# Optimization experiments

Hardware: AMD Instinct MI355X
Metric: run time of the kernel (lower is better)

Reference implementation:

```python
import jax, jax.numpy as jnp
import numpy as np

B, D, N, F = 2048, 512, 100000, 64
NEG = -1000000.0


def setup_inputs() -> dict:
    key = jax.random.key(0)
    k1, k2, k3, k4 = jax.random.split(key, 4)
    q = jax.random.normal(k1, (B, D), dtype=jnp.float32)
    rhs = jax.random.normal(k2, (D, N), dtype=jnp.float32)
    queries = jax.random.randint(k3, (B, 3), 0, N, dtype=jnp.int64)
    filter_idx = jax.random.randint(k4, (B, F), 0, N, dtype=jnp.int64)
    return {"q": q, "rhs": rhs, "queries": queries, "filter_idx": filter_idx}


def reference(q, rhs, queries, filter_idx):
    # targets[i] = score of the true triple = q[i] . rhs[:, true_rhs[i]]
    true_rhs = queries[:, 2]                         # [B]
    targets = jnp.einsum('bd,bd->b', q, rhs[:, true_rhs].T)  # [B]

    scores = q @ rhs                                  # [B, N]

    # filtered ranking: mask out known true tails + the query's own tail
    rows = jnp.arange(scores.shape[0])[:, None]       # [B, 1]
    scores = scores.at[rows, filter_idx].set(NEG)
    scores = scores.at[jnp.arange(scores.shape[0]), true_rhs].set(NEG)

    # rank = 1 + number of candidates scoring >= the true triple
    ranks = 1.0 + jnp.sum((scores >= targets[:, None]).astype(jnp.float32), axis=1)
    return ranks
```

## Files before the change

kernel.cpp:

```cpp
#include <hip/hip_runtime.h>
#include <hip/hip_bf16.h>

#define B_ 2048
#define D_ 512
#define N_ 100000
#define F_ 64
#define NEGV (-1000000.0f)

typedef __bf16 bfx8 __attribute__((ext_vector_type(8)));
typedef float f32x4 __attribute__((ext_vector_type(4)));
typedef unsigned short u16x8 __attribute__((ext_vector_type(8)));

static __device__ __forceinline__ unsigned short f2bf(float f) {
  unsigned u = __float_as_uint(f);
  unsigned r = (u + 0x7fffu + ((u >> 16) & 1u)) >> 16;
  return (unsigned short)r;
}
static __device__ __forceinline__ float bf2f(unsigned short u) {
  return __uint_as_float(((unsigned)u) << 16);
}

static __device__ __forceinline__ void async_copy16(const void* g, void* l) {
  __builtin_amdgcn_global_load_lds((const __attribute__((address_space(1))) void*)g,
                                   (__attribute__((address_space(3))) void*)l, 16, 0, 0);
}

__global__ void targets_init(const float* __restrict__ q, const float* __restrict__ rhs,
                             const int* __restrict__ queries, float* __restrict__ targets,
                             float* __restrict__ out) {
  __shared__ float wsum[4];
  int b = blockIdx.x;
  int tid = threadIdx.x, lane = tid & 63, w = tid >> 6;
  int p = queries[b * 3 + 2];
  float s = 0.f;
  for (int d = tid; d < D_; d += 256) s += q[b * D_ + d] * rhs[(size_t)d * N_ + p];
  for (int off = 32; off; off >>= 1) s += __shfl_down(s, off, 64);
  if (lane == 0) wsum[w] = s;
  __syncthreads();
  if (tid == 0) {
    targets[b] = wsum[0] + wsum[1] + wsum[2] + wsum[3];
    out[b] = 1.0f;
  }
}

__global__ void convert_q(const float* __restrict__ q, unsigned short* __restrict__ qb) {
  int i = blockIdx.x * blockDim.x + threadIdx.x;
  const float4* q4 = (const float4*)q;
  float4 v = q4[i];
  ushort4 o;
  o.x = f2bf(v.x); o.y = f2bf(v.y); o.z = f2bf(v.z); o.w = f2bf(v.w);
  ((ushort4*)qb)[i] = o;
}

__global__ void transpose_rhs(const float* __restrict__ rhs, unsigned short* __restrict__ rt) {
  __shared__ float tile[64][65];
  int n0 = blockIdx.x * 64, d0 = blockIdx.y * 64;
  int c = threadIdx.x & 63, r4 = threadIdx.x >> 6;
#pragma unroll
  for (int p = 0; p < 16; ++p) {
    int d = r4 + p * 4;
    int n = n0 + c;
    if (n < N_) tile[d][c] = rhs[(size_t)(d0 + d) * N_ + n];
  }
  __syncthreads();
#pragma unroll
  for (int p = 0; p < 4; ++p) {
    int e = p * 256 + threadIdx.x;
    int n = e >> 4, dg = e & 15;
    if (n0 + n < N_) {
      ushort4 o;
      o.x = f2bf(tile[dg * 4 + 0][n]);
      o.y = f2bf(tile[dg * 4 + 1][n]);
      o.z = f2bf(tile[dg * 4 + 2][n]);
      o.w = f2bf(tile[dg * 4 + 3][n]);
      *(ushort4*)(rt + (size_t)(n0 + n) * D_ + d0 + dg * 4) = o;
    }
  }
}

__global__ void __launch_bounds__(256) gemm_count(
    const unsigned short* __restrict__ qb,
    const unsigned short* __restrict__ rt,
    const float* __restrict__ targets,
    float* __restrict__ out) {
  __shared__ unsigned short As[128 * 32];
  __shared__ unsigned short Bs[128 * 32];
  __shared__ float sT[128];
  __shared__ int cnt[128];

  int tid = threadIdx.x;
  int m0 = blockIdx.x * 128;
  int n0 = blockIdx.y * 128;

  if (tid < 128) { sT[tid] = targets[m0 + tid]; cnt[tid] = 0; }

  int w = tid >> 6, lane = tid & 63;
  int mw = (w & 1) * 64, nw = (w >> 1) * 64;
  int quad = lane >> 4, l16 = lane & 15;

  f32x4 acc[4][4];
  f32x4 z = {0.f, 0.f, 0.f, 0.f};
#pragma unroll
  for (int i = 0; i < 4; ++i)
#pragma unroll
    for (int j = 0; j < 4; ++j) acc[i][j] = z;

  for (int kt = 0; kt < 16; ++kt) {
    int k0 = kt * 32;
    __syncthreads();
#pragma unroll
    for (int i = 0; i < 2; ++i) {
      int c = i * 256 + tid;
      int m = c >> 2, jj = c & 3;
      int j = jj ^ (m & 3);
      const unsigned short* gp = qb + (size_t)(m0 + m) * D_ + k0 + j * 8;
      async_copy16(gp, As + c * 8);
    }
#pragma unroll
    for (int i = 0; i < 2; ++i) {
      int c = i * 256 + tid;
      int n = c >> 2, jj = c & 3;
      int j = jj ^ (n & 3);
      int ng = n0 + n; if (ng > N_ - 1) ng = N_ - 1;
      const unsigned short* gp = rt + (size_t)ng * D_ + k0 + j * 8;
      async_copy16(gp, Bs + c * 8);
    }
    __syncthreads();

    bfx8 a[4], b[4];
#pragma unroll
    for (int mi = 0; mi < 4; ++mi) {
      int m = mw + mi * 16 + l16;
      int slot = m * 4 + (quad ^ (m & 3));
      u16x8 au = *(const u16x8*)(As + slot * 8);
      a[mi] = __builtin_bit_cast(bfx8, au);
    }
#pragma unroll
    for (int ni = 0; ni < 4; ++ni) {
      int n = nw + ni * 16 + l16;
      int slot = n * 4 + (quad ^ (n & 3));
      u16x8 bu = *(const u16x8*)(Bs + slot * 8);
      b[ni] = __builtin_bit_cast(bfx8, bu);
    }
#pragma unroll
    for (int mi = 0; mi < 4; ++mi)
#pragma unroll
      for (int ni = 0; ni < 4; ++ni)
        acc[mi][ni] = __builtin_amdgcn_mfma_f32_16x16x32_bf16(a[mi], b[ni], acc[mi][ni], 0, 0, 0);
  }

#pragma unroll
  for (int mi = 0; mi < 4; ++mi) {
#pragma unroll
    for (int reg = 0; reg < 4; ++reg) {
      int rl = mw + mi * 16 + quad * 4 + reg;
      float t = sT[rl];
      int c = 0;
#pragma unroll
      for (int ni = 0; ni < 4; ++ni) {
        int col = n0 + nw + ni * 16 + l16;
        if (col < N_ && acc[mi][ni][reg] >= t) c++;
      }
      if (c) atomicAdd(&cnt[rl], c);
    }
  }
  __syncthreads();
  if (tid < 128 && cnt[tid]) atomicAdd(&out[m0 + tid], (float)cnt[tid]);
}

__global__ void corrections(const unsigned short* __restrict__ qb,
                            const unsigned short* __restrict__ rt,
                            const int* __restrict__ queries,
                            const int* __restrict__ filt,
                            const float* __restrict__ targets,
                            float* __restrict__ out) {
  int b = blockIdx.x;
  int tid = threadIdx.x;
  int w = tid >> 6, lane = tid & 63;
  __shared__ int idx[F_ + 1];
  if (tid < F_) idx[tid] = filt[b * F_ + tid];
  if (tid == F_) idx[F_] = queries[b * 3 + 2];
  __syncthreads();
  float t = targets[b];
  float corr = 0.f;
  const u16x8* qrow = (const u16x8*)(qb + (size_t)b * D_);
  for (int ii = w; ii <= F_; ii += 4) {
    int p = idx[ii];
    bool uniq = true;
    for (int j = 0; j < ii; ++j)
      if (idx[j] == p) uniq = false;
    if (uniq) {
      u16x8 qv = qrow[lane];
      u16x8 rv = ((const u16x8*)(rt + (size_t)p * D_))[lane];
      float s = 0.f;
#pragma unroll
      for (int j = 0; j < 8; ++j) s += bf2f(qv[j]) * bf2f(rv[j]);
      for (int off = 32; off; off >>= 1) s += __shfl_down(s, off, 64);
      if (lane == 0)
        corr += (NEGV >= t ? 1.f : 0.f) - (s >= t ? 1.f : 0.f);
    }
  }
  if (lane == 0 && corr != 0.f) atomicAdd(&out[b], corr);
}

__global__ void fallback_count(const float* __restrict__ q, const float* __restrict__ rhs,
                               const int* __restrict__ queries, const int* __restrict__ filt,
                               const float* __restrict__ targets, float* __restrict__ out) {
  int b = blockIdx.y;
  int n = blockIdx.x * 256 + threadIdx.x;
  __shared__ float qs[D_];
  __shared__ int idx[F_ + 1];
  __shared__ int cnt;
  for (int d = threadIdx.x; d < D_; d += 256) qs[d] = q[b * D_ + d];
  if (threadIdx.x < F_) idx[threadIdx.x] = filt[b * F_ + threadIdx.x];
  if (threadIdx.x == F_) idx[F_] = queries[b * 3 + 2];
  if (threadIdx.x == 0) cnt = 0;
  __syncthreads();
  if (n < N_) {
    float t = targets[b];
    float s = 0.f;
    for (int d = 0; d < D_; ++d) s += qs[d] * rhs[(size_t)d * N_ + n];
    bool member = false;
    for (int j = 0; j <= F_; ++j)
      if (idx[j] == n) member = true;
    float sv = member ? NEGV : s;
    if (sv >= t) atomicAdd(&cnt, 1);
  }
  __syncthreads();
  if (threadIdx.x == 0 && cnt) atomicAdd(&out[b], (float)cnt);
}

extern "C" void kernel_launch(void* const* d_in, const int* in_sizes, int n_in,
                              void* d_out, int out_size, void* d_ws, size_t ws_size,
                              hipStream_t stream) {
  const float* q = (const float*)d_in[0];
  const float* rhs = (const float*)d_in[1];
  const int* queries = (const int*)d_in[2];
  const int* filt = (const int*)d_in[3];
  float* out = (float*)d_out;

  char* wsb = (char*)d_ws;
  float* targets = (float*)wsb;
  unsigned short* qb = (unsigned short*)(wsb + 8192);
  unsigned short* rt = (unsigned short*)(wsb + 8192 + (size_t)B_ * D_ * 2);
  size_t need = 8192 + (size_t)B_ * D_ * 2 + (size_t)N_ * D_ * 2;

  targets_init<<<B_, 256, 0, stream>>>(q, rhs, queries, targets, out);

  if (ws_size >= need) {
    convert_q<<<(B_ * D_ / 4) / 256, 256, 0, stream>>>(q, qb);
    transpose_rhs<<<dim3((N_ + 63) / 64, D_ / 64), 256, 0, stream>>>(rhs, rt);
    gemm_count<<<dim3(B_ / 128, (N_ + 127) / 128), 256, 0, stream>>>(qb, rt, targets, out);
    corrections<<<B_, 256, 0, stream>>>(qb, rt, queries, filt, targets, out);
  } else {
    fallback_count<<<dim3((N_ + 255) / 256, B_), 256, 0, stream>>>(q, rhs, queries, filt, targets, out);
  }
}
```

Measured before the change: 663.3 us.

## Double GEMM K-tile, vectorize transpose loads, shuffle-reduce counts, parallelize corrections

The GEMM K tile grows from 32 to 64, which halves the number of barrier-separated load stages. The XOR swizzle on the LDS layout is dropped, so A and B fragment reads now use a plain 128-byte row stride and may suffer LDS bank conflicts. Per-row counts are reduced with wave shuffles instead of LDS atomics. The transpose kernel uses float4 global loads for full tiles. The corrections kernel computes filter uniqueness in parallel once, hoists the q-row load and launches 512 threads.

```diff
diff --git a/kernel.cpp b/kernel.cpp
--- a/kernel.cpp
+++ b/kernel.cpp
@@ -55,17 +55,28 @@
 __global__ void transpose_rhs(const float* __restrict__ rhs, unsigned short* __restrict__ rt) {
   __shared__ float tile[64][65];
   int n0 = blockIdx.x * 64, d0 = blockIdx.y * 64;
-  int c = threadIdx.x & 63, r4 = threadIdx.x >> 6;
-#pragma unroll
-  for (int p = 0; p < 16; ++p) {
-    int d = r4 + p * 4;
-    int n = n0 + c;
-    if (n < N_) tile[d][c] = rhs[(size_t)(d0 + d) * N_ + n];
+  int tid = threadIdx.x;
+  if (n0 + 64 <= N_) {
+#pragma unroll
+    for (int p = 0; p < 4; ++p) {
+      int e = p * 256 + tid;
+      int d = e >> 4, c4 = e & 15;
+      float4 v = *(const float4*)(rhs + (size_t)(d0 + d) * N_ + n0 + c4 * 4);
+      tile[d][c4 * 4 + 0] = v.x; tile[d][c4 * 4 + 1] = v.y;
+      tile[d][c4 * 4 + 2] = v.z; tile[d][c4 * 4 + 3] = v.w;
+    }
+  } else {
+    int c = tid & 63, r4 = tid >> 6;
+#pragma unroll
+    for (int p = 0; p < 16; ++p) {
+      int d = r4 + p * 4;
+      if (n0 + c < N_) tile[d][c] = rhs[(size_t)(d0 + d) * N_ + n0 + c];
+    }
   }
   __syncthreads();
 #pragma unroll
   for (int p = 0; p < 4; ++p) {
-    int e = p * 256 + threadIdx.x;
+    int e = p * 256 + tid;
     int n = e >> 4, dg = e & 15;
     if (n0 + n < N_) {
       ushort4 o;
@@ -83,16 +94,16 @@
     const unsigned short* __restrict__ rt,
     const float* __restrict__ targets,
     float* __restrict__ out) {
-  __shared__ unsigned short As[128 * 32];
-  __shared__ unsigned short Bs[128 * 32];
+  __shared__ unsigned short As[128 * 64];
+  __shared__ unsigned short Bs[128 * 64];
   __shared__ float sT[128];
-  __shared__ int cnt[128];
+  __shared__ int cnt2[2][128];
 
   int tid = threadIdx.x;
   int m0 = blockIdx.x * 128;
   int n0 = blockIdx.y * 128;
 
-  if (tid < 128) { sT[tid] = targets[m0 + tid]; cnt[tid] = 0; }
+  if (tid < 128) sT[tid] = targets[m0 + tid];
 
   int w = tid >> 6, lane = tid & 63;
   int mw = (w & 1) * 64, nw = (w >> 1) * 64;
@@ -105,48 +116,47 @@
 #pragma unroll
     for (int j = 0; j < 4; ++j) acc[i][j] = z;
 
-  for (int kt = 0; kt < 16; ++kt) {
-    int k0 = kt * 32;
+  for (int kt = 0; kt < 8; ++kt) {
+    int k0 = kt * 64;
     __syncthreads();
 #pragma unroll
-    for (int i = 0; i < 2; ++i) {
+    for (int i = 0; i < 4; ++i) {
       int c = i * 256 + tid;
-      int m = c >> 2, jj = c & 3;
-      int j = jj ^ (m & 3);
-      const unsigned short* gp = qb + (size_t)(m0 + m) * D_ + k0 + j * 8;
+      int m = c >> 3, jj = c & 7;
+      const unsigned short* gp = qb + (size_t)(m0 + m) * D_ + k0 + jj * 8;
       async_copy16(gp, As + c * 8);
     }
 #pragma unroll
-    for (int i = 0; i < 2; ++i) {
+    for (int i = 0; i < 4; ++i) {
       int c = i * 256 + tid;
-      int n = c >> 2, jj = c & 3;
-      int j = jj ^ (n & 3);
+      int n = c >> 3, jj = c & 7;
       int ng = n0 + n; if (ng > N_ - 1) ng = N_ - 1;
-      const unsigned short* gp = rt + (size_t)ng * D_ + k0 + j * 8;
+      const unsigned short* gp = rt + (size_t)ng * D_ + k0 + jj * 8;
       async_copy16(gp, Bs + c * 8);
     }
     __syncthreads();
 
-    bfx8 a[4], b[4];
-#pragma unroll
-    for (int mi = 0; mi < 4; ++mi) {
-      int m = mw + mi * 16 + l16;
-      int slot = m * 4 + (quad ^ (m & 3));
-      u16x8 au = *(const u16x8*)(As + slot * 8);
-      a[mi] = __builtin_bit_cast(bfx8, au);
-    }
-#pragma unroll
-    for (int ni = 0; ni < 4; ++ni) {
-      int n = nw + ni * 16 + l16;
-      int slot = n * 4 + (quad ^ (n & 3));
-      u16x8 bu = *(const u16x8*)(Bs + slot * 8);
-      b[ni] = __builtin_bit_cast(bfx8, bu);
-    }
-#pragma unroll
-    for (int mi = 0; mi < 4; ++mi)
-#pragma unroll
-      for (int ni = 0; ni < 4; ++ni)
-        acc[mi][ni] = __builtin_amdgcn_mfma_f32_16x16x32_bf16(a[mi], b[ni], acc[mi][ni], 0, 0, 0);
+#pragma unroll
+    for (int kh = 0; kh < 2; ++kh) {
+      bfx8 a[4], b[4];
+#pragma unroll
+      for (int mi = 0; mi < 4; ++mi) {
+        int m = mw + mi * 16 + l16;
+        u16x8 au = *(const u16x8*)(As + m * 64 + kh * 32 + quad * 8);
+        a[mi] = __builtin_bit_cast(bfx8, au);
+      }
+#pragma unroll
+      for (int ni = 0; ni < 4; ++ni) {
+        int n = nw + ni * 16 + l16;
+        u16x8 bu = *(const u16x8*)(Bs + n * 64 + kh * 32 + quad * 8);
+        b[ni] = __builtin_bit_cast(bfx8, bu);
+      }
+#pragma unroll
+      for (int mi = 0; mi < 4; ++mi)
+#pragma unroll
+        for (int ni = 0; ni < 4; ++ni)
+          acc[mi][ni] = __builtin_amdgcn_mfma_f32_16x16x32_bf16(a[mi], b[ni], acc[mi][ni], 0, 0, 0);
+    }
   }
 
 #pragma unroll
@@ -161,11 +171,18 @@
         int col = n0 + nw + ni * 16 + l16;
         if (col < N_ && acc[mi][ni][reg] >= t) c++;
       }
-      if (c) atomicAdd(&cnt[rl], c);
-    }
-  }
-  __syncthreads();
-  if (tid < 128 && cnt[tid]) atomicAdd(&out[m0 + tid], (float)cnt[tid]);
+      c += __shfl_xor(c, 1, 64);
+      c += __shfl_xor(c, 2, 64);
+      c += __shfl_xor(c, 4, 64);
+      c += __shfl_xor(c, 8, 64);
+      if (l16 == 0) cnt2[w >> 1][rl] = c;
+    }
+  }
+  __syncthreads();
+  if (tid < 128) {
+    int tot = cnt2[0][tid] + cnt2[1][tid];
+    if (tot) atomicAdd(&out[m0 + tid], (float)tot);
+  }
 }
 
 __global__ void corrections(const unsigned short* __restrict__ qb,
@@ -178,27 +195,30 @@
   int tid = threadIdx.x;
   int w = tid >> 6, lane = tid & 63;
   __shared__ int idx[F_ + 1];
-  if (tid < F_) idx[tid] = filt[b * F_ + tid];
-  if (tid == F_) idx[F_] = queries[b * 3 + 2];
+  __shared__ unsigned char uq[F_ + 1];
+  if (tid <= F_) idx[tid] = (tid < F_) ? filt[b * F_ + tid] : queries[b * 3 + 2];
+  __syncthreads();
+  if (tid <= F_) {
+    int p = idx[tid];
+    bool u = true;
+    for (int j = 0; j < tid; ++j)
+      if (idx[j] == p) u = false;
+    uq[tid] = u;
+  }
   __syncthreads();
   float t = targets[b];
   float corr = 0.f;
-  const u16x8* qrow = (const u16x8*)(qb + (size_t)b * D_);
-  for (int ii = w; ii <= F_; ii += 4) {
+  u16x8 qv = ((const u16x8*)(qb + (size_t)b * D_))[lane];
+  for (int ii = w; ii <= F_; ii += 8) {
+    if (!uq[ii]) continue;
     int p = idx[ii];
-    bool uniq = true;
-    for (int j = 0; j < ii; ++j)
-      if (idx[j] == p) uniq = false;
-    if (uniq) {
-      u16x8 qv = qrow[lane];
-      u16x8 rv = ((const u16x8*)(rt + (size_t)p * D_))[lane];
-      float s = 0.f;
-#pragma unroll
-      for (int j = 0; j < 8; ++j) s += bf2f(qv[j]) * bf2f(rv[j]);
-      for (int off = 32; off; off >>= 1) s += __shfl_down(s, off, 64);
-      if (lane == 0)
-        corr += (NEGV >= t ? 1.f : 0.f) - (s >= t ? 1.f : 0.f);
-    }
+    u16x8 rv = ((const u16x8*)(rt + (size_t)p * D_))[lane];
+    float s = 0.f;
+#pragma unroll
+    for (int j = 0; j < 8; ++j) s += bf2f(qv[j]) * bf2f(rv[j]);
+    for (int off = 32; off; off >>= 1) s += __shfl_down(s, off, 64);
+    if (lane == 0)
+      corr += (NEGV >= t ? 1.f : 0.f) - (s >= t ? 1.f : 0.f);
   }
   if (lane == 0 && corr != 0.f) atomicAdd(&out[b], corr);
 }
@@ -251,7 +271,7 @@
     convert_q<<<(B_ * D_ / 4) / 256, 256, 0, stream>>>(q, qb);
     transpose_rhs<<<dim3((N_ + 63) / 64, D_ / 64), 256, 0, stream>>>(rhs, rt);
     gemm_count<<<dim3(B_ / 128, (N_ + 127) / 128), 256, 0, stream>>>(qb, rt, targets, out);
-    corrections<<<B_, 256, 0, stream>>>(qb, rt, queries, filt, targets, out);
+    corrections<<<B_, 512, 0, stream>>>(qb, rt, queries, filt, targets, out);
   } else {
     fallback_count<<<dim3((N_ + 255) / 256, B_), 256, 0, stream>>>(q, rhs, queries, filt, targets, out);
   }
```

After: 736.5 us. +11.0%, slower.
